# Kernel optimization log

Measured on AMD Instinct MI355X. Metric: run time of the kernel, lower is better.

## Reference

```python
import jax, jax.numpy as jnp
import numpy as np

B, N = 64, 512
D_ENT, H = 2000, 768
LN_EPS = 1e-12


def setup_inputs() -> dict:
    key = jax.random.key(0)
    ks = jax.random.split(key, 16)
    s = 1.0 / np.sqrt(D_ENT)
    sh = 1.0 / np.sqrt(H)
    return {
        "node_embeddings": jax.random.normal(ks[0], (B, N, D_ENT), jnp.float32),
        "node_types": jax.random.randint(ks[1], (B, N), 0, 2),
        "layers": jax.random.randint(ks[2], (B, N), 0, 8),
        "operators": jax.random.randint(ks[3], (B, N), 0, 2),
        "in_degs": jax.random.randint(ks[4], (B, N), 0, 8),
        "out_degs": jax.random.randint(ks[5], (B, N), 0, 8),
        "negs": jax.random.randint(ks[6], (B, N), 0, 2),
        "type_emb": jax.random.normal(ks[7], (2, H), jnp.float32),
        "layer_emb": jax.random.normal(ks[8], (8, H), jnp.float32),
        "op_emb": jax.random.normal(ks[9], (2, H), jnp.float32),
        "in_emb": jax.random.normal(ks[10], (8, H), jnp.float32),
        "out_emb": jax.random.normal(ks[11], (8, H), jnp.float32),
        "proj_w": jax.random.uniform(ks[12], (H, D_ENT), jnp.float32, -s, s),
        "proj_b": jnp.zeros((H,), jnp.float32),
        "neg_w": jax.random.uniform(ks[13], (H, H), jnp.float32, -sh, sh),
        "neg_b": jnp.zeros((H,), jnp.float32),
        "ln_g": jnp.ones((H,), jnp.float32),
        "ln_b": jnp.zeros((H,), jnp.float32),
    }


def reference(node_embeddings, node_types, layers, operators, in_degs, out_degs, negs,
              type_emb, layer_emb, op_emb, in_emb, out_emb,
              proj_w, proj_b, neg_w, neg_b, ln_g, ln_b):
    # linear projection: [B,N,D_ENT] @ [D_ENT,H]
    x = jnp.einsum("bnd,hd->bnh", node_embeddings, proj_w) + proj_b
    # summed small-table lookups
    x = x + type_emb[node_types] + layer_emb[layers] + op_emb[operators] \
        + in_emb[in_degs] + out_emb[out_degs]
    # rows with negs==1 go through MLP (single Linear h->h); masked select/scatter
    y = jnp.einsum("bnh,gh->bng", x, neg_w) + neg_b
    x = jnp.where((negs == 1)[..., None], y, x)
    # LayerNorm
    mu = jnp.mean(x, axis=-1, keepdims=True)
    var = jnp.mean(jnp.square(x - mu), axis=-1, keepdims=True)
    x = (x - mu) * jax.lax.rsqrt(var + LN_EPS) * ln_g + ln_b
    # dropout is identity in eval mode
    return x
```

## Files before the change

kernel.cpp:

```cpp
#include <hip/hip_runtime.h>
#include <stdint.h>

typedef unsigned short u16;
typedef short v8s __attribute__((ext_vector_type(8)));
typedef float v4f __attribute__((ext_vector_type(4)));

typedef __attribute__((address_space(1))) uint32_t g_u32;
typedef __attribute__((address_space(3))) uint32_t l_u32;

__device__ __forceinline__ void glds16(const void* g, void* l) {
    __builtin_amdgcn_global_load_lds((const g_u32*)g, (l_u32*)l, 16, 0, 0);
}

__device__ __forceinline__ u16 f2b(float f) {
    uint32_t u = __builtin_bit_cast(uint32_t, f);
    u += 0x7FFFu + ((u >> 16) & 1u);
    return (u16)(u >> 16);
}

__device__ __forceinline__ uint32_t pk2(float a, float b) {
    uint32_t ua = __builtin_bit_cast(uint32_t, a) + 0x8000u;
    uint32_t ub = __builtin_bit_cast(uint32_t, b) + 0x8000u;
    return __builtin_amdgcn_perm(ub, ua, 0x07060302u);
}

#define MTOT  32768
#define HDIM  768
#define KDIM  2000
#define KPAD  2016

__global__ __launch_bounds__(256) void cvt_weights(
    const float* __restrict__ pw, const float* __restrict__ nw,
    u16* __restrict__ Wb, u16* __restrict__ NWb)
{
    const int h = blockIdx.x;
    const float* src = pw + (size_t)h * KDIM;
    u16* dst = Wb + (size_t)h * KPAD;
    for (int k = threadIdx.x; k < KPAD; k += 256)
        dst[k] = (k < KDIM) ? f2b(src[k]) : (u16)0;
    const float* s2 = nw + (size_t)h * HDIM;
    u16* d2 = NWb + (size_t)h * HDIM;
    for (int k = threadIdx.x; k < HDIM; k += 256)
        d2[k] = f2b(s2[k]);
}

__global__ __launch_bounds__(256, 2) void gemm1(
    const float* __restrict__ A, const u16* __restrict__ Wb,
    const float* __restrict__ pb,
    const int* __restrict__ i_ty, const int* __restrict__ i_la,
    const int* __restrict__ i_op, const int* __restrict__ i_in, const int* __restrict__ i_ou,
    const float* __restrict__ te, const float* __restrict__ le, const float* __restrict__ oe,
    const float* __restrict__ ie, const float* __restrict__ ooe,
    u16* __restrict__ Xb)
{
    __shared__ __align__(16) float Asf[3][128 * 32];
    __shared__ __align__(16) u16  Bs[3][128 * 32];

    const int bid = blockIdx.x;
    const int slot = bid >> 3;
    const int mt = (bid & 7) * 32 + slot / 6;
    const int nt = slot % 6;
    const int m_base = mt * 128, n_base = nt * 128;

    const int tid = threadIdx.x;
    const int w = tid >> 6, lane = tid & 63;
    const int lm = lane & 15, quad = lane >> 4;
    const int wm = (w >> 1) * 64, wn = (w & 1) * 64;

    const float* aRowBase[4];
    int aOff[4];
    int aBase[4];
#pragma unroll
    for (int t = 0; t < 4; t++) {
        const int rl = w * 32 + t * 8 + (lane >> 3);
        const int c16 = (lane & 7) ^ (rl & 7);
        aRowBase[t] = A + (size_t)(m_base + rl) * KDIM;
        aOff[t] = c16 * 4;
        aBase[t] = (w * 32 + t * 8) * 32;
    }
    const u16* bSrc[2];
    int bBase[2];
#pragma unroll
    for (int t = 0; t < 2; t++) {
        const int rl = w * 32 + t * 16 + (lane >> 2);
        const int c = (lane & 3) ^ ((rl >> 1) & 3);
        bSrc[t] = Wb + (size_t)(n_base + rl) * KPAD + c * 8;
        bBase[t] = (w * 32 + t * 16) * 32;
    }

    v4f acc[4][4];
#pragma unroll
    for (int i = 0; i < 4; i++)
#pragma unroll
        for (int j = 0; j < 4; j++) acc[i][j] = (v4f){0.f, 0.f, 0.f, 0.f};

    auto issue = [&](int kb) {
        const int sl = kb % 3;
#pragma unroll
        for (int t = 0; t < 4; t++) {
            int k = kb * 32 + aOff[t];
            k = (k > 1996) ? 1996 : k;
            glds16(aRowBase[t] + k, &Asf[sl][aBase[t]]);
        }
#pragma unroll
        for (int t = 0; t < 2; t++)
            glds16(bSrc[t] + kb * 32, &Bs[sl][bBase[t]]);
    };

    auto compute = [&](int kb) {
        const int sl = kb % 3;
        v8s af[4], bf[4];
#pragma unroll
        for (int i = 0; i < 4; i++) {
            const int r = wm + i * 16 + lm;
            const int sw = r & 7;
            const float4 lo = *(const float4*)&Asf[sl][r * 32 + (((2 * quad)     ^ sw) << 2)];
            const float4 hi = *(const float4*)&Asf[sl][r * 32 + (((2 * quad + 1) ^ sw) << 2)];
            int4 p;
            p.x = (int)pk2(lo.x, lo.y); p.y = (int)pk2(lo.z, lo.w);
            p.z = (int)pk2(hi.x, hi.y); p.w = (int)pk2(hi.z, hi.w);
            af[i] = __builtin_bit_cast(v8s, p);
        }
#pragma unroll
        for (int j = 0; j < 4; j++) {
            const int r = wn + j * 16 + lm;
            bf[j] = *(const v8s*)&Bs[sl][r * 32 + ((quad ^ ((r >> 1) & 3)) << 3)];
        }
#pragma unroll
        for (int i = 0; i < 4; i++)
#pragma unroll
            for (int j = 0; j < 4; j++)
                acc[i][j] = __builtin_amdgcn_mfma_f32_16x16x32_bf16(af[i], bf[j], acc[i][j], 0, 0, 0);
    };

    issue(0);
    issue(1);

    for (int kb = 0; kb < 61; ++kb) {
        asm volatile("s_waitcnt vmcnt(6)" ::: "memory");
        __builtin_amdgcn_s_barrier();
        __builtin_amdgcn_sched_barrier(0);
        issue(kb + 2);
        compute(kb);
    }
    asm volatile("s_waitcnt vmcnt(6)" ::: "memory");
    __builtin_amdgcn_s_barrier();
    __builtin_amdgcn_sched_barrier(0);
    compute(61);
    asm volatile("s_waitcnt vmcnt(0)" ::: "memory");
    __builtin_amdgcn_s_barrier();
    __builtin_amdgcn_sched_barrier(0);
    compute(62);

#pragma unroll
    for (int i = 0; i < 4; i++) {
#pragma unroll
        for (int r = 0; r < 4; r++) {
            const int row = m_base + wm + i * 16 + quad * 4 + r;
            const int ty = i_ty[row], la = i_la[row], op = i_op[row];
            const int di = i_in[row], doo = i_ou[row];
            const float* pte = te + (size_t)ty * HDIM;
            const float* ple = le + (size_t)la * HDIM;
            const float* poe = oe + (size_t)op * HDIM;
            const float* pie = ie + (size_t)di * HDIM;
            const float* pou = ooe + (size_t)doo * HDIM;
            u16* orow = Xb + (size_t)row * HDIM;
#pragma unroll
            for (int j = 0; j < 4; j++) {
                const int col = n_base + wn + j * 16 + lm;
                float v = acc[i][j][r] + pb[col] + pte[col] + ple[col] + poe[col] + pie[col] + pou[col];
                orow[col] = f2b(v);
            }
        }
    }
}

__global__ __launch_bounds__(256, 3) void gemm2(
    const u16* __restrict__ Xb, const u16* __restrict__ NWb,
    const float* __restrict__ nb, u16* __restrict__ Yb)
{
    __shared__ __align__(16) u16 As[3][128 * 32];
    __shared__ __align__(16) u16 Bs[3][128 * 32];

    const int bid = blockIdx.x;
    const int slot = bid >> 3;
    const int mt = (bid & 7) * 32 + slot / 6;
    const int nt = slot % 6;
    const int m_base = mt * 128, n_base = nt * 128;

    const int tid = threadIdx.x;
    const int w = tid >> 6, lane = tid & 63;
    const int lm = lane & 15, quad = lane >> 4;
    const int wm = (w >> 1) * 64, wn = (w & 1) * 64;

    const u16* aSrc[2];
    const u16* bSrc[2];
    int sBase[2];
#pragma unroll
    for (int t = 0; t < 2; t++) {
        const int rl = w * 32 + t * 16 + (lane >> 2);
        const int c = (lane & 3) ^ ((rl >> 1) & 3);
        aSrc[t] = Xb  + (size_t)(m_base + rl) * HDIM + c * 8;
        bSrc[t] = NWb + (size_t)(n_base + rl) * HDIM + c * 8;
        sBase[t] = (w * 32 + t * 16) * 32;
    }

    v4f acc[4][4];
#pragma unroll
    for (int i = 0; i < 4; i++)
#pragma unroll
        for (int j = 0; j < 4; j++) acc[i][j] = (v4f){0.f, 0.f, 0.f, 0.f};

    auto issue = [&](int kb) {
        const int sl = kb % 3;
#pragma unroll
        for (int t = 0; t < 2; t++) {
            glds16(aSrc[t] + kb * 32, &As[sl][sBase[t]]);
            glds16(bSrc[t] + kb * 32, &Bs[sl][sBase[t]]);
        }
    };

    auto compute = [&](int kb) {
        const int sl = kb % 3;
        v8s af[4], bf[4];
#pragma unroll
        for (int i = 0; i < 4; i++) {
            const int r = wm + i * 16 + lm;
            af[i] = *(const v8s*)&As[sl][r * 32 + ((quad ^ ((r >> 1) & 3)) << 3)];
        }
#pragma unroll
        for (int j = 0; j < 4; j++) {
            const int r = wn + j * 16 + lm;
            bf[j] = *(const v8s*)&Bs[sl][r * 32 + ((quad ^ ((r >> 1) & 3)) << 3)];
        }
#pragma unroll
        for (int i = 0; i < 4; i++)
#pragma unroll
            for (int j = 0; j < 4; j++)
                acc[i][j] = __builtin_amdgcn_mfma_f32_16x16x32_bf16(af[i], bf[j], acc[i][j], 0, 0, 0);
    };

    issue(0);
    issue(1);

    for (int kb = 0; kb < 22; ++kb) {
        asm volatile("s_waitcnt vmcnt(4)" ::: "memory");
        __builtin_amdgcn_s_barrier();
        __builtin_amdgcn_sched_barrier(0);
        issue(kb + 2);
        compute(kb);
    }
    asm volatile("s_waitcnt vmcnt(4)" ::: "memory");
    __builtin_amdgcn_s_barrier();
    __builtin_amdgcn_sched_barrier(0);
    compute(22);
    asm volatile("s_waitcnt vmcnt(0)" ::: "memory");
    __builtin_amdgcn_s_barrier();
    __builtin_amdgcn_sched_barrier(0);
    compute(23);

#pragma unroll
    for (int i = 0; i < 4; i++) {
#pragma unroll
        for (int r = 0; r < 4; r++) {
            const int row = m_base + wm + i * 16 + quad * 4 + r;
            u16* orow = Yb + (size_t)row * HDIM;
#pragma unroll
            for (int j = 0; j < 4; j++) {
                const int col = n_base + wn + j * 16 + lm;
                orow[col] = f2b(acc[i][j][r] + nb[col]);
            }
        }
    }
}

__global__ __launch_bounds__(256) void ln_k(
    const u16* __restrict__ Xb, const u16* __restrict__ Yb,
    const int* __restrict__ negs,
    const float* __restrict__ g, const float* __restrict__ b,
    float* __restrict__ out)
{
    const int w = threadIdx.x >> 6, lane = threadIdx.x & 63;
    const int row = blockIdx.x * 4 + w;
    const u16* src = ((negs[row] == 1) ? Yb : Xb) + (size_t)row * HDIM;

    float v[12];
    float s = 0.f, ss = 0.f;
#pragma unroll
    for (int p = 0; p < 3; p++) {
        uint2 u = *(const uint2*)(src + (p * 64 + lane) * 4);
        float f0 = __builtin_bit_cast(float, u.x << 16);
        float f1 = __builtin_bit_cast(float, u.x & 0xFFFF0000u);
        float f2 = __builtin_bit_cast(float, u.y << 16);
        float f3 = __builtin_bit_cast(float, u.y & 0xFFFF0000u);
        v[p * 4 + 0] = f0; v[p * 4 + 1] = f1; v[p * 4 + 2] = f2; v[p * 4 + 3] = f3;
        s += f0 + f1 + f2 + f3;
        ss += f0 * f0 + f1 * f1 + f2 * f2 + f3 * f3;
    }
#pragma unroll
    for (int off = 1; off < 64; off <<= 1) {
        s += __shfl_xor(s, off);
        ss += __shfl_xor(ss, off);
    }
    const float mean = s * (1.f / (float)HDIM);
    const float var = ss * (1.f / (float)HDIM) - mean * mean;
    const float rs = rsqrtf(var + 1e-12f);

    float* orow = out + (size_t)row * HDIM;
#pragma unroll
    for (int p = 0; p < 3; p++) {
        const int c0 = (p * 64 + lane) * 4;
        float4 gg = *(const float4*)(g + c0);
        float4 bb = *(const float4*)(b + c0);
        float4 o;
        o.x = (v[p * 4 + 0] - mean) * rs * gg.x + bb.x;
        o.y = (v[p * 4 + 1] - mean) * rs * gg.y + bb.y;
        o.z = (v[p * 4 + 2] - mean) * rs * gg.z + bb.z;
        o.w = (v[p * 4 + 3] - mean) * rs * gg.w + bb.w;
        *(float4*)(orow + c0) = o;
    }
}

extern "C" void kernel_launch(void* const* d_in, const int* in_sizes, int n_in,
                              void* d_out, int out_size, void* d_ws, size_t ws_size,
                              hipStream_t stream) {
    (void)in_sizes; (void)n_in; (void)out_size; (void)ws_size;
    const float* A   = (const float*)d_in[0];
    const int* i_ty  = (const int*)d_in[1];
    const int* i_la  = (const int*)d_in[2];
    const int* i_op  = (const int*)d_in[3];
    const int* i_in  = (const int*)d_in[4];
    const int* i_ou  = (const int*)d_in[5];
    const int* negs  = (const int*)d_in[6];
    const float* te  = (const float*)d_in[7];
    const float* le  = (const float*)d_in[8];
    const float* oe  = (const float*)d_in[9];
    const float* ie  = (const float*)d_in[10];
    const float* ooe = (const float*)d_in[11];
    const float* pw  = (const float*)d_in[12];
    const float* pb  = (const float*)d_in[13];
    const float* nw  = (const float*)d_in[14];
    const float* nb  = (const float*)d_in[15];
    const float* lng = (const float*)d_in[16];
    const float* lnb = (const float*)d_in[17];
    float* out = (float*)d_out;

    char* ws = (char*)d_ws;
    u16* Wb  = (u16*)ws;
    u16* NWb = (u16*)(ws + 3096576);
    u16* Xb  = (u16*)(ws + 3096576 + 1179648);
    u16* Yb  = (u16*)(ws + 3096576 + 1179648 + 50331648);

    cvt_weights<<<768, 256, 0, stream>>>(pw, nw, Wb, NWb);
    gemm1<<<1536, 256, 0, stream>>>(A, Wb, pb, i_ty, i_la, i_op, i_in, i_ou,
                                    te, le, oe, ie, ooe, Xb);
    gemm2<<<1536, 256, 0, stream>>>(Xb, NWb, nb, Yb);
    ln_k<<<8192, 256, 0, stream>>>(Xb, Yb, negs, lng, lnb, out);
}
```

Measured before the change: 730.0 us.

## Use full-width 128x768 tiles with 1024-thread blocks so A is read once

Both GEMMs switch from 128x128 tiles with 1536 blocks of 256 threads to one 128x768 tile per block with 1024 threads (16 waves), so each A row tile is fetched only once instead of six times. In gemm1, fp32 A is loaded into registers, converted to bf16 and written to LDS once, rather than converted on every fragment read. The pipeline moves from a triple-buffered async LDS load to double buffering with extra barriers. This cuts repeated global traffic on the large fp32 input, but the grid drops to 256 blocks (about one per CU), with fewer blocks to hide latency and more register and LDS pressure per block.

```diff
diff --git a/kernel.cpp b/kernel.cpp
--- a/kernel.cpp
+++ b/kernel.cpp
@@ -44,7 +44,7 @@
         d2[k] = f2b(s2[k]);
 }
 
-__global__ __launch_bounds__(256, 2) void gemm1(
+__global__ __launch_bounds__(1024) void gemm1(
     const float* __restrict__ A, const u16* __restrict__ Wb,
     const float* __restrict__ pb,
     const int* __restrict__ i_ty, const int* __restrict__ i_la,
@@ -53,101 +53,110 @@
     const float* __restrict__ ie, const float* __restrict__ ooe,
     u16* __restrict__ Xb)
 {
-    __shared__ __align__(16) float Asf[3][128 * 32];
-    __shared__ __align__(16) u16  Bs[3][128 * 32];
-
-    const int bid = blockIdx.x;
-    const int slot = bid >> 3;
-    const int mt = (bid & 7) * 32 + slot / 6;
-    const int nt = slot % 6;
-    const int m_base = mt * 128, n_base = nt * 128;
+    __shared__ __align__(16) u16 As[2][128 * 32];
+    __shared__ __align__(16) u16 Bs[2][768 * 32];
 
     const int tid = threadIdx.x;
     const int w = tid >> 6, lane = tid & 63;
     const int lm = lane & 15, quad = lane >> 4;
-    const int wm = (w >> 1) * 64, wn = (w & 1) * 64;
-
-    const float* aRowBase[4];
-    int aOff[4];
-    int aBase[4];
-#pragma unroll
-    for (int t = 0; t < 4; t++) {
-        const int rl = w * 32 + t * 8 + (lane >> 3);
-        const int c16 = (lane & 7) ^ (rl & 7);
-        aRowBase[t] = A + (size_t)(m_base + rl) * KDIM;
-        aOff[t] = c16 * 4;
-        aBase[t] = (w * 32 + t * 8) * 32;
-    }
-    const u16* bSrc[2];
-    int bBase[2];
-#pragma unroll
-    for (int t = 0; t < 2; t++) {
-        const int rl = w * 32 + t * 16 + (lane >> 2);
-        const int c = (lane & 3) ^ ((rl >> 1) & 3);
-        bSrc[t] = Wb + (size_t)(n_base + rl) * KPAD + c * 8;
-        bBase[t] = (w * 32 + t * 16) * 32;
-    }
-
-    v4f acc[4][4];
+    const int wm = (w >> 3) * 64, wn = (w & 7) * 96;
+    const int m_base = blockIdx.x * 128;
+
+    const int rA = w * 8 + (lane >> 3);
+    const int cA = lane & 7;
+    const float* aRow = A + (size_t)(m_base + rA) * KDIM;
+    const int aW = rA * 32 + (((cA >> 1) ^ ((rA >> 1) & 3)) << 3) + ((cA & 1) << 2);
+
+    const u16* bSrc[3];
+    int bDst[3];
+#pragma unroll
+    for (int t = 0; t < 3; t++) {
+        const int rB = w * 48 + t * 16 + (lane >> 2);
+        const int cB = (lane & 3) ^ ((rB >> 1) & 3);
+        bSrc[t] = Wb + (size_t)rB * KPAD + cB * 8;
+        bDst[t] = (w * 48 + t * 16) * 32;
+    }
+
+    v4f acc[4][6];
 #pragma unroll
     for (int i = 0; i < 4; i++)
 #pragma unroll
-        for (int j = 0; j < 4; j++) acc[i][j] = (v4f){0.f, 0.f, 0.f, 0.f};
-
-    auto issue = [&](int kb) {
-        const int sl = kb % 3;
-#pragma unroll
-        for (int t = 0; t < 4; t++) {
-            int k = kb * 32 + aOff[t];
-            k = (k > 1996) ? 1996 : k;
-            glds16(aRowBase[t] + k, &Asf[sl][aBase[t]]);
-        }
-#pragma unroll
-        for (int t = 0; t < 2; t++)
-            glds16(bSrc[t] + kb * 32, &Bs[sl][bBase[t]]);
-    };
-
+        for (int j = 0; j < 6; j++) acc[i][j] = (v4f){0.f, 0.f, 0.f, 0.f};
+
+    auto lda = [&](int kb) -> float4 {
+        int kf = kb * 32 + cA * 4;
+        kf = (kf > 1996) ? 1996 : kf;
+        return *(const float4*)(aRow + kf);
+    };
+    auto wrA = [&](float4 a, int sl) {
+        uint2 p;
+        p.x = pk2(a.x, a.y);
+        p.y = pk2(a.z, a.w);
+        *(uint2*)&As[sl][aW] = p;
+    };
+    auto issueB = [&](int kb) {
+        const int sl = kb & 1;
+#pragma unroll
+        for (int t = 0; t < 3; t++)
+            glds16(bSrc[t] + kb * 32, &Bs[sl][bDst[t]]);
+    };
     auto compute = [&](int kb) {
-        const int sl = kb % 3;
-        v8s af[4], bf[4];
+        const int sl = kb & 1;
+        v8s af[4], bf[6];
 #pragma unroll
         for (int i = 0; i < 4; i++) {
             const int r = wm + i * 16 + lm;
-            const int sw = r & 7;
-            const float4 lo = *(const float4*)&Asf[sl][r * 32 + (((2 * quad)     ^ sw) << 2)];
-            const float4 hi = *(const float4*)&Asf[sl][r * 32 + (((2 * quad + 1) ^ sw) << 2)];
-            int4 p;
-            p.x = (int)pk2(lo.x, lo.y); p.y = (int)pk2(lo.z, lo.w);
-            p.z = (int)pk2(hi.x, hi.y); p.w = (int)pk2(hi.z, hi.w);
-            af[i] = __builtin_bit_cast(v8s, p);
-        }
-#pragma unroll
-        for (int j = 0; j < 4; j++) {
+            af[i] = *(const v8s*)&As[sl][r * 32 + ((quad ^ ((r >> 1) & 3)) << 3)];
+        }
+#pragma unroll
+        for (int j = 0; j < 6; j++) {
             const int r = wn + j * 16 + lm;
             bf[j] = *(const v8s*)&Bs[sl][r * 32 + ((quad ^ ((r >> 1) & 3)) << 3)];
         }
 #pragma unroll
         for (int i = 0; i < 4; i++)
 #pragma unroll
-            for (int j = 0; j < 4; j++)
+            for (int j = 0; j < 6; j++)
                 acc[i][j] = __builtin_amdgcn_mfma_f32_16x16x32_bf16(af[i], bf[j], acc[i][j], 0, 0, 0);
     };
 
-    issue(0);
-    issue(1);
-
+    float4 aP = lda(0);
+    __builtin_amdgcn_sched_barrier(0);
+    issueB(0);
+    float4 aN = lda(1);
+    __builtin_amdgcn_sched_barrier(0);
+    issueB(1);
+    asm volatile("s_waitcnt vmcnt(7)" ::: "memory");
+    wrA(aP, 0);
+    aP = aN;
+
+#pragma unroll 2
     for (int kb = 0; kb < 61; ++kb) {
-        asm volatile("s_waitcnt vmcnt(6)" ::: "memory");
+        asm volatile("s_waitcnt vmcnt(4)" ::: "memory");
+        asm volatile("s_waitcnt lgkmcnt(0)" ::: "memory");
         __builtin_amdgcn_s_barrier();
         __builtin_amdgcn_sched_barrier(0);
-        issue(kb + 2);
         compute(kb);
-    }
-    asm volatile("s_waitcnt vmcnt(6)" ::: "memory");
+        __builtin_amdgcn_sched_barrier(0);
+        __builtin_amdgcn_s_barrier();
+        aN = lda(kb + 2);
+        __builtin_amdgcn_sched_barrier(0);
+        issueB(kb + 2);
+        asm volatile("s_waitcnt vmcnt(7)" ::: "memory");
+        wrA(aP, (kb + 1) & 1);
+        aP = aN;
+    }
+    asm volatile("s_waitcnt vmcnt(4)" ::: "memory");
+    asm volatile("s_waitcnt lgkmcnt(0)" ::: "memory");
     __builtin_amdgcn_s_barrier();
     __builtin_amdgcn_sched_barrier(0);
     compute(61);
+    __builtin_amdgcn_sched_barrier(0);
+    __builtin_amdgcn_s_barrier();
+    asm volatile("s_waitcnt vmcnt(3)" ::: "memory");
+    wrA(aP, 0);
     asm volatile("s_waitcnt vmcnt(0)" ::: "memory");
+    asm volatile("s_waitcnt lgkmcnt(0)" ::: "memory");
     __builtin_amdgcn_s_barrier();
     __builtin_amdgcn_sched_barrier(0);
     compute(62);
@@ -166,8 +175,8 @@
             const float* pou = ooe + (size_t)doo * HDIM;
             u16* orow = Xb + (size_t)row * HDIM;
 #pragma unroll
-            for (int j = 0; j < 4; j++) {
-                const int col = n_base + wn + j * 16 + lm;
+            for (int j = 0; j < 6; j++) {
+                const int col = wn + j * 16 + lm;
                 float v = acc[i][j][r] + pb[col] + pte[col] + ple[col] + poe[col] + pie[col] + pou[col];
                 orow[col] = f2b(v);
             }
@@ -175,85 +184,86 @@
     }
 }
 
-__global__ __launch_bounds__(256, 3) void gemm2(
+__global__ __launch_bounds__(1024) void gemm2(
     const u16* __restrict__ Xb, const u16* __restrict__ NWb,
     const float* __restrict__ nb, u16* __restrict__ Yb)
 {
-    __shared__ __align__(16) u16 As[3][128 * 32];
-    __shared__ __align__(16) u16 Bs[3][128 * 32];
-
-    const int bid = blockIdx.x;
-    const int slot = bid >> 3;
-    const int mt = (bid & 7) * 32 + slot / 6;
-    const int nt = slot % 6;
-    const int m_base = mt * 128, n_base = nt * 128;
+    __shared__ __align__(16) u16 As[2][128 * 32];
+    __shared__ __align__(16) u16 Bs[2][768 * 32];
 
     const int tid = threadIdx.x;
     const int w = tid >> 6, lane = tid & 63;
     const int lm = lane & 15, quad = lane >> 4;
-    const int wm = (w >> 1) * 64, wn = (w & 1) * 64;
-
-    const u16* aSrc[2];
-    const u16* bSrc[2];
-    int sBase[2];
-#pragma unroll
-    for (int t = 0; t < 2; t++) {
-        const int rl = w * 32 + t * 16 + (lane >> 2);
-        const int c = (lane & 3) ^ ((rl >> 1) & 3);
-        aSrc[t] = Xb  + (size_t)(m_base + rl) * HDIM + c * 8;
-        bSrc[t] = NWb + (size_t)(n_base + rl) * HDIM + c * 8;
-        sBase[t] = (w * 32 + t * 16) * 32;
-    }
-
-    v4f acc[4][4];
+    const int wm = (w >> 3) * 64, wn = (w & 7) * 96;
+    const int m_base = blockIdx.x * 128;
+
+    const int rA = (w & 7) * 16 + (lane >> 2);
+    const int cA = (lane & 3) ^ ((rA >> 1) & 3);
+    const u16* aSrc = Xb + (size_t)(m_base + rA) * HDIM + cA * 8;
+    const int aDst = ((w & 7) * 16) * 32;
+
+    const u16* bSrc[3];
+    int bDst[3];
+#pragma unroll
+    for (int t = 0; t < 3; t++) {
+        const int rB = w * 48 + t * 16 + (lane >> 2);
+        const int cB = (lane & 3) ^ ((rB >> 1) & 3);
+        bSrc[t] = NWb + (size_t)rB * HDIM + cB * 8;
+        bDst[t] = (w * 48 + t * 16) * 32;
+    }
+
+    v4f acc[4][6];
 #pragma unroll
     for (int i = 0; i < 4; i++)
 #pragma unroll
-        for (int j = 0; j < 4; j++) acc[i][j] = (v4f){0.f, 0.f, 0.f, 0.f};
+        for (int j = 0; j < 6; j++) acc[i][j] = (v4f){0.f, 0.f, 0.f, 0.f};
 
     auto issue = [&](int kb) {
-        const int sl = kb % 3;
-#pragma unroll
-        for (int t = 0; t < 2; t++) {
-            glds16(aSrc[t] + kb * 32, &As[sl][sBase[t]]);
-            glds16(bSrc[t] + kb * 32, &Bs[sl][sBase[t]]);
-        }
-    };
-
+        const int sl = kb & 1;
+        glds16(aSrc + kb * 32, &As[sl][aDst]);
+#pragma unroll
+        for (int t = 0; t < 3; t++)
+            glds16(bSrc[t] + kb * 32, &Bs[sl][bDst[t]]);
+    };
     auto compute = [&](int kb) {
-        const int sl = kb % 3;
-        v8s af[4], bf[4];
+        const int sl = kb & 1;
+        v8s af[4], bf[6];
 #pragma unroll
         for (int i = 0; i < 4; i++) {
             const int r = wm + i * 16 + lm;
             af[i] = *(const v8s*)&As[sl][r * 32 + ((quad ^ ((r >> 1) & 3)) << 3)];
         }
 #pragma unroll
-        for (int j = 0; j < 4; j++) {
+        for (int j = 0; j < 6; j++) {
             const int r = wn + j * 16 + lm;
             bf[j] = *(const v8s*)&Bs[sl][r * 32 + ((quad ^ ((r >> 1) & 3)) << 3)];
         }
 #pragma unroll
         for (int i = 0; i < 4; i++)
 #pragma unroll
-            for (int j = 0; j < 4; j++)
+            for (int j = 0; j < 6; j++)
                 acc[i][j] = __builtin_amdgcn_mfma_f32_16x16x32_bf16(af[i], bf[j], acc[i][j], 0, 0, 0);
     };
 
     issue(0);
     issue(1);
 
+#pragma unroll 2
     for (int kb = 0; kb < 22; ++kb) {
         asm volatile("s_waitcnt vmcnt(4)" ::: "memory");
         __builtin_amdgcn_s_barrier();
         __builtin_amdgcn_sched_barrier(0);
+        compute(kb);
+        __builtin_amdgcn_sched_barrier(0);
+        __builtin_amdgcn_s_barrier();
         issue(kb + 2);
-        compute(kb);
     }
     asm volatile("s_waitcnt vmcnt(4)" ::: "memory");
     __builtin_amdgcn_s_barrier();
     __builtin_amdgcn_sched_barrier(0);
     compute(22);
+    __builtin_amdgcn_sched_barrier(0);
+    __builtin_amdgcn_s_barrier();
     asm volatile("s_waitcnt vmcnt(0)" ::: "memory");
     __builtin_amdgcn_s_barrier();
     __builtin_amdgcn_sched_barrier(0);
@@ -266,8 +276,8 @@
             const int row = m_base + wm + i * 16 + quad * 4 + r;
             u16* orow = Yb + (size_t)row * HDIM;
 #pragma unroll
-            for (int j = 0; j < 4; j++) {
-                const int col = n_base + wn + j * 16 + lm;
+            for (int j = 0; j < 6; j++) {
+                const int col = wn + j * 16 + lm;
                 orow[col] = f2b(acc[i][j][r] + nb[col]);
             }
         }
@@ -352,8 +362,8 @@
     u16* Yb  = (u16*)(ws + 3096576 + 1179648 + 50331648);
 
     cvt_weights<<<768, 256, 0, stream>>>(pw, nw, Wb, NWb);
-    gemm1<<<1536, 256, 0, stream>>>(A, Wb, pb, i_ty, i_la, i_op, i_in, i_ou,
+    gemm1<<<256, 1024, 0, stream>>>(A, Wb, pb, i_ty, i_la, i_op, i_in, i_ou,
                                     te, le, oe, ie, ooe, Xb);
-    gemm2<<<1536, 256, 0, stream>>>(Xb, NWb, nb, Yb);
+    gemm2<<<256, 1024, 0, stream>>>(Xb, NWb, nb, Yb);
     ln_k<<<8192, 256, 0, stream>>>(Xb, Yb, negs, lng, lnb, out);
 }
```

Measured after the change: 1.167 ms. 59.8% more time.

## Compact negs rows for second GEMM and retile GEMMs to 128x256 with 512 threads

Applied to the files above, without the earlier changes.

Adds a single-block compaction kernel that gathers the indices of rows with negs==1, so the second GEMM only processes those rows, gathering Xb rows via cmap and skipping tiles past the count. The layer norm then reads Y through a position map. Both GEMMs move to 512-thread blocks with 128x256 tiles and double buffering, where the old code used triple buffering, and the barrier/wait ordering changes. The cost is an extra serial launch (the compaction runs on one block) and possibly less load latency hiding with only two buffers.

```diff
diff --git a/kernel.cpp b/kernel.cpp
--- a/kernel.cpp
+++ b/kernel.cpp
@@ -11,13 +11,11 @@
 __device__ __forceinline__ void glds16(const void* g, void* l) {
     __builtin_amdgcn_global_load_lds((const g_u32*)g, (l_u32*)l, 16, 0, 0);
 }
-
 __device__ __forceinline__ u16 f2b(float f) {
     uint32_t u = __builtin_bit_cast(uint32_t, f);
     u += 0x7FFFu + ((u >> 16) & 1u);
     return (u16)(u >> 16);
 }
-
 __device__ __forceinline__ uint32_t pk2(float a, float b) {
     uint32_t ua = __builtin_bit_cast(uint32_t, a) + 0x8000u;
     uint32_t ub = __builtin_bit_cast(uint32_t, b) + 0x8000u;
@@ -28,6 +26,9 @@
 #define HDIM  768
 #define KDIM  2000
 #define KPAD  2016
+
+#define VMW(n) asm volatile("s_waitcnt vmcnt(" #n ")" ::: "memory")
+#define BARX do { __builtin_amdgcn_s_barrier(); __builtin_amdgcn_sched_barrier(0); } while (0)
 
 __global__ __launch_bounds__(256) void cvt_weights(
     const float* __restrict__ pw, const float* __restrict__ nw,
@@ -44,7 +45,35 @@
         d2[k] = f2b(s2[k]);
 }
 
-__global__ __launch_bounds__(256, 2) void gemm1(
+__global__ __launch_bounds__(256) void compact_k(
+    const int* __restrict__ negs, int* __restrict__ cmap,
+    int* __restrict__ pos, int* __restrict__ cnt)
+{
+    __shared__ int pref[257];
+    const int t = threadIdx.x;
+    const int base = t * 128;
+    int c = 0;
+    for (int j = 0; j < 128; j++) c += (negs[base + j] == 1);
+    __shared__ int wsum[256];
+    wsum[t] = c;
+    __syncthreads();
+    if (t == 0) {
+        int a = 0;
+        for (int i = 0; i < 256; i++) { pref[i] = a; a += wsum[i]; }
+        pref[256] = a;
+        cnt[0] = a;
+    }
+    __syncthreads();
+    int off = pref[t];
+    for (int j = 0; j < 128; j++) {
+        const int r = base + j;
+        if (negs[r] == 1) { cmap[off] = r; pos[r] = off; off++; }
+    }
+    const int total = pref[256];
+    for (int j = total + t; j < MTOT; j += 256) cmap[j] = 0;
+}
+
+__global__ __launch_bounds__(512, 4) void gemm1(
     const float* __restrict__ A, const u16* __restrict__ Wb,
     const float* __restrict__ pb,
     const int* __restrict__ i_ty, const int* __restrict__ i_la,
@@ -53,30 +82,27 @@
     const float* __restrict__ ie, const float* __restrict__ ooe,
     u16* __restrict__ Xb)
 {
-    __shared__ __align__(16) float Asf[3][128 * 32];
-    __shared__ __align__(16) u16  Bs[3][128 * 32];
+    __shared__ __align__(16) float Asf[2][128 * 32];
+    __shared__ __align__(16) u16  Bs[2][256 * 32];
 
     const int bid = blockIdx.x;
-    const int slot = bid >> 3;
-    const int mt = (bid & 7) * 32 + slot / 6;
-    const int nt = slot % 6;
-    const int m_base = mt * 128, n_base = nt * 128;
+    const int sw = (bid & 7) * 96 + (bid >> 3);
+    const int mt = sw / 3, nt = sw % 3;
+    const int m_base = mt * 128, n_base = nt * 256;
 
     const int tid = threadIdx.x;
     const int w = tid >> 6, lane = tid & 63;
     const int lm = lane & 15, quad = lane >> 4;
-    const int wm = (w >> 1) * 64, wn = (w & 1) * 64;
-
-    const float* aRowBase[4];
-    int aOff[4];
-    int aBase[4];
-#pragma unroll
-    for (int t = 0; t < 4; t++) {
-        const int rl = w * 32 + t * 8 + (lane >> 3);
-        const int c16 = (lane & 7) ^ (rl & 7);
+    const int wm = (w >> 2) * 64, wn = (w & 3) * 64;
+
+    const float* aRowBase[2];
+    int aOff[2], aBase[2];
+#pragma unroll
+    for (int t = 0; t < 2; t++) {
+        const int rl = w * 16 + t * 8 + (lane >> 3);
         aRowBase[t] = A + (size_t)(m_base + rl) * KDIM;
-        aOff[t] = c16 * 4;
-        aBase[t] = (w * 32 + t * 8) * 32;
+        aOff[t] = ((lane & 7) ^ (rl & 7)) * 4;
+        aBase[t] = (w * 16 + t * 8) * 32;
     }
     const u16* bSrc[2];
     int bBase[2];
@@ -95,9 +121,9 @@
         for (int j = 0; j < 4; j++) acc[i][j] = (v4f){0.f, 0.f, 0.f, 0.f};
 
     auto issue = [&](int kb) {
-        const int sl = kb % 3;
-#pragma unroll
-        for (int t = 0; t < 4; t++) {
+        const int sl = kb & 1;
+#pragma unroll
+        for (int t = 0; t < 2; t++) {
             int k = kb * 32 + aOff[t];
             k = (k > 1996) ? 1996 : k;
             glds16(aRowBase[t] + k, &Asf[sl][aBase[t]]);
@@ -106,16 +132,15 @@
         for (int t = 0; t < 2; t++)
             glds16(bSrc[t] + kb * 32, &Bs[sl][bBase[t]]);
     };
-
     auto compute = [&](int kb) {
-        const int sl = kb % 3;
+        const int sl = kb & 1;
         v8s af[4], bf[4];
 #pragma unroll
         for (int i = 0; i < 4; i++) {
             const int r = wm + i * 16 + lm;
-            const int sw = r & 7;
-            const float4 lo = *(const float4*)&Asf[sl][r * 32 + (((2 * quad)     ^ sw) << 2)];
-            const float4 hi = *(const float4*)&Asf[sl][r * 32 + (((2 * quad + 1) ^ sw) << 2)];
+            const int s8 = r & 7;
+            const float4 lo = *(const float4*)&Asf[sl][r * 32 + (((2 * quad)     ^ s8) << 2)];
+            const float4 hi = *(const float4*)&Asf[sl][r * 32 + (((2 * quad + 1) ^ s8) << 2)];
             int4 p;
             p.x = (int)pk2(lo.x, lo.y); p.y = (int)pk2(lo.z, lo.w);
             p.z = (int)pk2(hi.x, hi.y); p.w = (int)pk2(hi.z, hi.w);
@@ -137,20 +162,17 @@
     issue(1);
 
     for (int kb = 0; kb < 61; ++kb) {
-        asm volatile("s_waitcnt vmcnt(6)" ::: "memory");
-        __builtin_amdgcn_s_barrier();
+        VMW(4);
+        BARX;
+        compute(kb);
         __builtin_amdgcn_sched_barrier(0);
+        BARX;
         issue(kb + 2);
-        compute(kb);
-    }
-    asm volatile("s_waitcnt vmcnt(6)" ::: "memory");
-    __builtin_amdgcn_s_barrier();
+    }
+    VMW(4); BARX; compute(61);
     __builtin_amdgcn_sched_barrier(0);
-    compute(61);
-    asm volatile("s_waitcnt vmcnt(0)" ::: "memory");
-    __builtin_amdgcn_s_barrier();
-    __builtin_amdgcn_sched_barrier(0);
-    compute(62);
+    BARX;
+    VMW(0); BARX; compute(62);
 
 #pragma unroll
     for (int i = 0; i < 4; i++) {
@@ -175,34 +197,37 @@
     }
 }
 
-__global__ __launch_bounds__(256, 3) void gemm2(
+__global__ __launch_bounds__(512, 4) void gemm2(
     const u16* __restrict__ Xb, const u16* __restrict__ NWb,
-    const float* __restrict__ nb, u16* __restrict__ Yb)
-{
-    __shared__ __align__(16) u16 As[3][128 * 32];
-    __shared__ __align__(16) u16 Bs[3][128 * 32];
+    const float* __restrict__ nb, const int* __restrict__ cmap,
+    const int* __restrict__ cnt, u16* __restrict__ Yb)
+{
+    __shared__ __align__(16) u16 As[2][128 * 32];
+    __shared__ __align__(16) u16 Bs[2][256 * 32];
 
     const int bid = blockIdx.x;
-    const int slot = bid >> 3;
-    const int mt = (bid & 7) * 32 + slot / 6;
-    const int nt = slot % 6;
-    const int m_base = mt * 128, n_base = nt * 128;
+    const int sw = (bid & 7) * 96 + (bid >> 3);
+    const int mt = sw / 3, nt = sw % 3;
+    const int m_base = mt * 128, n_base = nt * 256;
+    if (m_base >= cnt[0]) return;
 
     const int tid = threadIdx.x;
     const int w = tid >> 6, lane = tid & 63;
     const int lm = lane & 15, quad = lane >> 4;
-    const int wm = (w >> 1) * 64, wn = (w & 1) * 64;
-
-    const u16* aSrc[2];
+    const int wm = (w >> 2) * 64, wn = (w & 3) * 64;
+
+    const int rlA = w * 16 + (lane >> 2);
+    const int cAx = (lane & 3) ^ ((rlA >> 1) & 3);
+    const u16* aSrc = Xb + (size_t)cmap[m_base + rlA] * HDIM + cAx * 8;
+    const int aBase = (w * 16) * 32;
     const u16* bSrc[2];
-    int sBase[2];
+    int bBase[2];
 #pragma unroll
     for (int t = 0; t < 2; t++) {
         const int rl = w * 32 + t * 16 + (lane >> 2);
         const int c = (lane & 3) ^ ((rl >> 1) & 3);
-        aSrc[t] = Xb  + (size_t)(m_base + rl) * HDIM + c * 8;
         bSrc[t] = NWb + (size_t)(n_base + rl) * HDIM + c * 8;
-        sBase[t] = (w * 32 + t * 16) * 32;
+        bBase[t] = (w * 32 + t * 16) * 32;
     }
 
     v4f acc[4][4];
@@ -212,16 +237,14 @@
         for (int j = 0; j < 4; j++) acc[i][j] = (v4f){0.f, 0.f, 0.f, 0.f};
 
     auto issue = [&](int kb) {
-        const int sl = kb % 3;
-#pragma unroll
-        for (int t = 0; t < 2; t++) {
-            glds16(aSrc[t] + kb * 32, &As[sl][sBase[t]]);
-            glds16(bSrc[t] + kb * 32, &Bs[sl][sBase[t]]);
-        }
+        const int sl = kb & 1;
+        glds16(aSrc + kb * 32, &As[sl][aBase]);
+#pragma unroll
+        for (int t = 0; t < 2; t++)
+            glds16(bSrc[t] + kb * 32, &Bs[sl][bBase[t]]);
     };
-
     auto compute = [&](int kb) {
-        const int sl = kb % 3;
+        const int sl = kb & 1;
         v8s af[4], bf[4];
 #pragma unroll
         for (int i = 0; i < 4; i++) {
@@ -244,27 +267,24 @@
     issue(1);
 
     for (int kb = 0; kb < 22; ++kb) {
-        asm volatile("s_waitcnt vmcnt(4)" ::: "memory");
-        __builtin_amdgcn_s_barrier();
+        VMW(3);
+        BARX;
+        compute(kb);
         __builtin_amdgcn_sched_barrier(0);
+        BARX;
         issue(kb + 2);
-        compute(kb);
-    }
-    asm volatile("s_waitcnt vmcnt(4)" ::: "memory");
-    __builtin_amdgcn_s_barrier();
+    }
+    VMW(3); BARX; compute(22);
     __builtin_amdgcn_sched_barrier(0);
-    compute(22);
-    asm volatile("s_waitcnt vmcnt(0)" ::: "memory");
-    __builtin_amdgcn_s_barrier();
-    __builtin_amdgcn_sched_barrier(0);
-    compute(23);
+    BARX;
+    VMW(0); BARX; compute(23);
 
 #pragma unroll
     for (int i = 0; i < 4; i++) {
 #pragma unroll
         for (int r = 0; r < 4; r++) {
-            const int row = m_base + wm + i * 16 + quad * 4 + r;
-            u16* orow = Yb + (size_t)row * HDIM;
+            const int crow = m_base + wm + i * 16 + quad * 4 + r;
+            u16* orow = Yb + (size_t)crow * HDIM;
 #pragma unroll
             for (int j = 0; j < 4; j++) {
                 const int col = n_base + wn + j * 16 + lm;
@@ -276,13 +296,14 @@
 
 __global__ __launch_bounds__(256) void ln_k(
     const u16* __restrict__ Xb, const u16* __restrict__ Yb,
-    const int* __restrict__ negs,
+    const int* __restrict__ negs, const int* __restrict__ pos,
     const float* __restrict__ g, const float* __restrict__ b,
     float* __restrict__ out)
 {
     const int w = threadIdx.x >> 6, lane = threadIdx.x & 63;
     const int row = blockIdx.x * 4 + w;
-    const u16* src = ((negs[row] == 1) ? Yb : Xb) + (size_t)row * HDIM;
+    const u16* src = (negs[row] == 1) ? (Yb + (size_t)pos[row] * HDIM)
+                                      : (Xb + (size_t)row * HDIM);
 
     float v[12];
     float s = 0.f, ss = 0.f;
@@ -348,12 +369,16 @@
     char* ws = (char*)d_ws;
     u16* Wb  = (u16*)ws;
     u16* NWb = (u16*)(ws + 3096576);
-    u16* Xb  = (u16*)(ws + 3096576 + 1179648);
-    u16* Yb  = (u16*)(ws + 3096576 + 1179648 + 50331648);
+    u16* Xb  = (u16*)(ws + 4276224);
+    u16* Yb  = (u16*)(ws + 4276224 + 50331648);
+    int* cmap = (int*)(ws + 4276224 + 100663296);
+    int* pos  = (int*)(ws + 4276224 + 100663296 + 131072);
+    int* cnt  = (int*)(ws + 4276224 + 100663296 + 262144);
 
     cvt_weights<<<768, 256, 0, stream>>>(pw, nw, Wb, NWb);
-    gemm1<<<1536, 256, 0, stream>>>(A, Wb, pb, i_ty, i_la, i_op, i_in, i_ou,
-                                    te, le, oe, ie, ooe, Xb);
-    gemm2<<<1536, 256, 0, stream>>>(Xb, NWb, nb, Yb);
-    ln_k<<<8192, 256, 0, stream>>>(Xb, Yb, negs, lng, lnb, out);
-}
+    compact_k<<<1, 256, 0, stream>>>(negs, cmap, pos, cnt);
+    gemm1<<<768, 512, 0, stream>>>(A, Wb, pb, i_ty, i_la, i_op, i_in, i_ou,
+                                   te, le, oe, ie, ooe, Xb);
+    gemm2<<<768, 512, 0, stream>>>(Xb, NWb, nb, cmap, cnt, Yb);
+    ln_k<<<8192, 256, 0, stream>>>(Xb, Yb, negs, pos, lng, lnb, out);
+}
```

Result: slower. 746.1 us (+2.2%).
